# Kernel tuning notes

Hardware: AMD Instinct MI355X
Metric: run time of the kernel (lower is better)

## Reference

```python
import jax, jax.numpy as jnp
import numpy as np

H = 16
D_MODEL = 1024
D_K = D_MODEL // H
NEG = -1e9


def setup_inputs() -> dict:
    key = jax.random.key(0)
    ks = jax.random.split(key, 12)
    B, S = 2, 2048
    inp = {
        "query": jax.random.normal(ks[0], (B, S, D_MODEL), jnp.float32),
        "key": jax.random.normal(ks[1], (B, S, D_MODEL), jnp.float32),
        "value": jax.random.normal(ks[2], (B, S, D_MODEL), jnp.float32),
        "mask": jnp.ones((B, 1, S), jnp.int32),
    }
    s = 1.0 / np.sqrt(D_MODEL)
    for i, nm in enumerate(["Wq", "Wk", "Wv", "Wo"]):
        inp[nm] = jax.random.normal(ks[3 + i], (D_MODEL, D_MODEL), jnp.float32) * s
        inp["b" + nm[1]] = jax.random.normal(ks[7 + i], (D_MODEL,), jnp.float32) * s
    return inp


def _split_heads(x):
    B, S, _ = x.shape
    return x.reshape(B, S, H, D_K).transpose(0, 2, 1, 3)  # [B,H,S,Dk]


def reference(query, key, value, mask, Wq, bq, Wk, bk, Wv, bv, Wo, bo):
    q = _split_heads(query @ Wq + bq)
    k = _split_heads(key @ Wk + bk)
    v = _split_heads(value @ Wv + bv)
    scores = jnp.einsum("bhqd,bhkd->bhqk", q, k) / jnp.sqrt(jnp.float32(D_K))
    # mask [B,1,Sk] -> broadcast as [B,1,1,Sk]
    scores = jnp.where(mask[:, None, :, :] == 0, NEG, scores)
    attn = jax.nn.softmax(scores, axis=-1)  # dropout is identity in eval mode
    out = jnp.einsum("bhqk,bhkd->bhqd", attn, v)
    B, _, Sq, _ = out.shape
    out = out.transpose(0, 2, 1, 3).reshape(B, Sq, H * D_K)
    return out @ Wo + bo
```

## Files before the change

### kernel.cpp

```cpp
#include <hip/hip_runtime.h>
#include <hip/hip_bf16.h>

typedef __attribute__((ext_vector_type(8))) short short8;
typedef __attribute__((ext_vector_type(4))) float float4v;
typedef __attribute__((ext_vector_type(2))) unsigned int uint2v;
typedef __hip_bfloat16 bf16;

#define MFMA16(a, b, c) __builtin_amdgcn_mfma_f32_16x16x32_bf16((a), (b), (c), 0, 0, 0)

static __device__ __forceinline__ short8 load8(const bf16* p) {
    return *reinterpret_cast<const short8*>(p);
}
static __device__ __forceinline__ unsigned short bfu(float x) {
    union { bf16 b; unsigned short u; } c; c.b = __float2bfloat16(x); return c.u;
}
static __device__ __forceinline__ unsigned pack2(float lo, float hi) {
    return ((unsigned)bfu(hi) << 16) | bfu(lo);
}
static __device__ __forceinline__ short bf_bits(float x) {
    union { bf16 b; short u; } c; c.b = __float2bfloat16(x); return c.u;
}
static __device__ __forceinline__ short8 cvt8(float4 a, float4 b) {
    short8 r;
    r[0] = bf_bits(a.x); r[1] = bf_bits(a.y); r[2] = bf_bits(a.z); r[3] = bf_bits(a.w);
    r[4] = bf_bits(b.x); r[5] = bf_bits(b.y); r[6] = bf_bits(b.z); r[7] = bf_bits(b.w);
    return r;
}

typedef const __attribute__((address_space(1))) unsigned int* gp1;
typedef __attribute__((address_space(3))) unsigned int* lp3;
static __device__ __forceinline__ void async16(const void* g, void* l) {
    __builtin_amdgcn_global_load_lds((gp1)g, (lp3)l, 16, 0, 0);
}

__global__ __launch_bounds__(256) void transpose_qkv(
    const float* __restrict__ Wq, const float* __restrict__ Wk,
    const float* __restrict__ Wv, bf16* __restrict__ out_base)
{
    __shared__ bf16 tile[64][65];
    const float* in = (blockIdx.z == 0) ? Wq : (blockIdx.z == 1) ? Wk : Wv;
    bf16* out = out_base + (size_t)blockIdx.z * 1048576;
    int tx = threadIdx.x, ty = threadIdx.y;
    int bx = blockIdx.x * 64, by = blockIdx.y * 64;
    for (int i = ty; i < 64; i += 4)
        tile[i][tx] = __float2bfloat16(in[(size_t)(by + i) * 1024 + bx + tx]);
    __syncthreads();
    for (int i = ty; i < 64; i += 4)
        out[(size_t)(bx + i) * 1024 + by + tx] = tile[tx][i];
}

__global__ __launch_bounds__(256) void transpose_one(
    const float* __restrict__ in, bf16* __restrict__ out)
{
    __shared__ bf16 tile[64][65];
    int tx = threadIdx.x, ty = threadIdx.y;
    int bx = blockIdx.x * 64, by = blockIdx.y * 64;
    for (int i = ty; i < 64; i += 4)
        tile[i][tx] = __float2bfloat16(in[(size_t)(by + i) * 1024 + bx + tx]);
    __syncthreads();
    for (int i = ty; i < 64; i += 4)
        out[(size_t)(bx + i) * 1024 + by + tx] = tile[tx][i];
}

__global__ __launch_bounds__(256, 3) void qkv_gemm(
    const float* __restrict__ Xq, const float* __restrict__ Xk,
    const float* __restrict__ Xv, const bf16* __restrict__ Wt_all,
    const float* __restrict__ bq, const float* __restrict__ bk,
    const float* __restrict__ bv,
    bf16* __restrict__ outq, bf16* __restrict__ outk, bf16* __restrict__ outv)
{
    __shared__ float As[128 * 64];
    __shared__ bf16  Bs[128 * 64];

    int wg = blockIdx.x;
    int xcd = wg & 7;
    int jj = wg >> 3;
    int grp = xcd * 12 + (jj >> 3);
    int z = grp >> 5;
    int m_blk = grp & 31;
    int n_blk = jj & 7;

    const float* X    = (z == 0) ? Xq : (z == 1) ? Xk : Xv;
    const float* bias = (z == 0) ? bq : (z == 1) ? bk : bv;
    const bf16*  Wt   = Wt_all + (size_t)z * 1048576;
    bf16*        out  = (z == 0) ? outq : (z == 1) ? outk : outv;
    bool vmode = (z == 2);

    int tid = threadIdx.x;
    int w = tid >> 6, lane = tid & 63, l16 = lane & 15, quad = lane >> 4;
    int m_base = m_blk * 128, n_base = n_blk * 128;

    int r4 = lane >> 4, s16 = lane & 15;
    int r8 = lane >> 3, s8 = lane & 7;
    const float* Asrc0 = X + (size_t)(m_base + w * 32 + r4) * 1024 + ((s16 ^ r4) << 2);
    const float* Asrc1 = X + (size_t)(m_base + w * 32 + r4) * 1024 + ((s16 ^ (4 + r4)) << 2);
    const bf16*  Bsrc  = Wt + (size_t)(n_base + w * 32 + r8) * 1024 + ((s8 ^ r8) << 3);

    int wm = (w & 1) * 64, wn = (w >> 1) * 64;
    int sw = l16 & 7;

    float4v zero = {0.f, 0.f, 0.f, 0.f};
    float4v acc[4][4];
    #pragma unroll
    for (int mi = 0; mi < 4; ++mi)
        #pragma unroll
        for (int nj = 0; nj < 4; ++nj) acc[mi][nj] = zero;

    for (int it = 0; it < 16; ++it) {
        int kt = it * 64;
        #pragma unroll
        for (int p = 0; p < 8; ++p) {
            const float* s = ((p & 1) ? Asrc1 : Asrc0) + (size_t)p * 4096 + kt;
            async16(s, (char*)As + (w * 32 + p * 4) * 256);
        }
        #pragma unroll
        for (int p = 0; p < 4; ++p)
            async16(Bsrc + (size_t)p * 8192 + kt, (char*)Bs + (w * 32 + p * 8) * 128);
        __syncthreads();

        #pragma unroll
        for (int kk = 0; kk < 2; ++kk) {
            short8 af[4], bfr[4];
            #pragma unroll
            for (int mi = 0; mi < 4; ++mi) {
                const float* rp = As + (wm + mi * 16 + l16) * 64;
                float4 f0 = *(const float4*)(rp + (((kk * 8 + quad * 2)     ^ sw) << 2));
                float4 f1 = *(const float4*)(rp + (((kk * 8 + quad * 2 + 1) ^ sw) << 2));
                af[mi] = cvt8(f0, f1);
            }
            #pragma unroll
            for (int nj = 0; nj < 4; ++nj) {
                const bf16* rp = Bs + (wn + nj * 16 + l16) * 64;
                bfr[nj] = load8(rp + (((kk * 4 + quad) ^ sw) << 3));
            }
            #pragma unroll
            for (int mi = 0; mi < 4; ++mi)
                #pragma unroll
                for (int nj = 0; nj < 4; ++nj)
                    acc[mi][nj] = MFMA16(af[mi], bfr[nj], acc[mi][nj]);
        }
        __syncthreads();
    }

    float bsv[4];
    #pragma unroll
    for (int nj = 0; nj < 4; ++nj)
        bsv[nj] = bias[n_base + wn + nj * 16 + l16];

    float qs = (z == 0) ? 0.18033688f : 1.0f;

    #pragma unroll
    for (int mi = 0; mi < 4; ++mi) {
        #pragma unroll
        for (int nj = 0; nj < 4; ++nj) {
            int n = n_base + wn + nj * 16 + l16;
            int h = n >> 6, dk = n & 63;
            int m0 = m_base + wm + mi * 16 + quad * 4;
            int b = m0 >> 11, s0 = m0 & 2047;
            if (vmode) {
                float v0 = acc[mi][nj][0] + bsv[nj];
                float v1 = acc[mi][nj][1] + bsv[nj];
                float v2 = acc[mi][nj][2] + bsv[nj];
                float v3 = acc[mi][nj][3] + bsv[nj];
                uint2 pv; pv.x = pack2(v0, v1); pv.y = pack2(v2, v3);
                size_t idx = ((size_t)(b * 16 + h) * 64 + dk) * 2048 + s0;
                *reinterpret_cast<uint2*>(out + idx) = pv;
            } else {
                #pragma unroll
                for (int r = 0; r < 4; ++r) {
                    size_t idx = (((size_t)(b * 16 + h) * 2048 + s0 + r) * 64 + dk);
                    out[idx] = __float2bfloat16((acc[mi][nj][r] + bsv[nj]) * qs);
                }
            }
        }
    }
}

__global__ __launch_bounds__(256, 2) void out_gemm(
    const bf16* __restrict__ A, const bf16* __restrict__ Wt,
    const float* __restrict__ bias, float* __restrict__ out)
{
    __shared__ bf16 As[128 * 128];
    __shared__ bf16 Bs[64 * 128];

    int wg = blockIdx.x;
    int xcd = wg & 7;
    int jj = wg >> 3;
    int m_blk = xcd * 4 + (jj >> 4);
    int n_blk = jj & 15;

    int tid = threadIdx.x;
    int w = tid >> 6, lane = tid & 63, l16 = lane & 15, quad = lane >> 4;
    int m_base = m_blk * 128, n_base = n_blk * 64;

    int r4 = lane >> 4, s16 = lane & 15;

    int wm = (w & 1) * 64, wn = (w >> 1) * 32;

    float4v zero = {0.f, 0.f, 0.f, 0.f};
    float4v acc[4][2];
    #pragma unroll
    for (int mi = 0; mi < 4; ++mi)
        #pragma unroll
        for (int nj = 0; nj < 2; ++nj) acc[mi][nj] = zero;

    for (int it = 0; it < 8; ++it) {
        int kt = it * 128;
        #pragma unroll
        for (int p = 0; p < 8; ++p) {
            int row = w * 32 + p * 4 + r4;
            const bf16* s = A + (size_t)(m_base + row) * 1024 + kt
                              + ((s16 ^ (row & 15)) << 3);
            async16(s, (char*)As + (w * 32 + p * 4) * 256);
        }
        #pragma unroll
        for (int p = 0; p < 4; ++p) {
            int row = w * 16 + p * 4 + r4;
            const bf16* s = Wt + (size_t)(n_base + row) * 1024 + kt
                              + ((s16 ^ (row & 15)) << 3);
            async16(s, (char*)Bs + (w * 16 + p * 4) * 256);
        }
        __syncthreads();

        #pragma unroll
        for (int kk = 0; kk < 4; ++kk) {
            short8 af[4], bfr[2];
            #pragma unroll
            for (int mi = 0; mi < 4; ++mi) {
                const bf16* rp = As + (wm + mi * 16 + l16) * 128;
                af[mi] = load8(rp + (((kk * 4 + quad) ^ l16) << 3));
            }
            #pragma unroll
            for (int nj = 0; nj < 2; ++nj) {
                const bf16* rp = Bs + (wn + nj * 16 + l16) * 128;
                bfr[nj] = load8(rp + (((kk * 4 + quad) ^ l16) << 3));
            }
            #pragma unroll
            for (int mi = 0; mi < 4; ++mi)
                #pragma unroll
                for (int nj = 0; nj < 2; ++nj)
                    acc[mi][nj] = MFMA16(af[mi], bfr[nj], acc[mi][nj]);
        }
        __syncthreads();
    }

    float bsv[2];
    #pragma unroll
    for (int nj = 0; nj < 2; ++nj)
        bsv[nj] = bias[n_base + wn + nj * 16 + l16];

    #pragma unroll
    for (int mi = 0; mi < 4; ++mi)
        #pragma unroll
        for (int nj = 0; nj < 2; ++nj) {
            int n = n_base + wn + nj * 16 + l16;
            int m0 = m_base + wm + mi * 16 + quad * 4;
            #pragma unroll
            for (int r = 0; r < 4; ++r)
                out[(size_t)(m0 + r) * 1024 + n] = acc[mi][nj][r] + bsv[nj];
        }
}

__global__ __launch_bounds__(512, 4) void attn_fused(
    const bf16* __restrict__ Qm, const bf16* __restrict__ Km,
    const bf16* __restrict__ Vt, const int* __restrict__ mask,
    bf16* __restrict__ Oout)
{
    __shared__ __align__(16) bf16 Kc[3][64 * 64];
    __shared__ __align__(16) bf16 Vc[3][64 * 64];
    __shared__ unsigned long long maskb[32];

    int tid = threadIdx.x;
    int w = tid >> 6, lane = tid & 63, l16 = lane & 15, quad = lane >> 4;
    int wg = blockIdx.x;
    int xcd = wg & 7;
    int jj = wg >> 3;
    int bh = xcd * 4 + (jj >> 4);
    int qg = jj & 15;
    int b = bh >> 4, h = bh & 15;
    int qt = qg * 8 + w;

    const int* mb = mask + b * 2048;
    #pragma unroll
    for (int i = 0; i < 4; ++i) {
        unsigned long long bal = __ballot(mb[w * 256 + i * 64 + lane] != 0);
        if (lane == 0) maskb[w * 4 + i] = bal;
    }

    const bf16* Qb = Qm + ((size_t)bh * 2048 + (size_t)qt * 16) * 64;
    short8 bQ0 = load8(Qb + l16 * 64 + quad * 8);
    short8 bQ1 = load8(Qb + l16 * 64 + 32 + quad * 8);

    int r8 = lane >> 3, s8 = lane & 7;
    const bf16* Ksrc = Km + (size_t)bh * 131072 + (size_t)(w * 8 + r8) * 64 + ((s8 ^ r8) << 3);
    const bf16* Vsrc = Vt + (size_t)bh * 131072 + (size_t)(w * 8 + r8) * 2048 + ((s8 ^ r8) << 3);

    int sw = l16 & 7;

    float4v zero = {0.f, 0.f, 0.f, 0.f};
    float4v Oacc[4];
    #pragma unroll
    for (int g = 0; g < 4; ++g) Oacc[g] = zero;
    float lsum = 0.f;

    async16(Ksrc,        (char*)&Kc[0][0] + w * 1024);
    async16(Vsrc,        (char*)&Vc[0][0] + w * 1024);
    async16(Ksrc + 4096, (char*)&Kc[1][0] + w * 1024);
    async16(Vsrc + 64,   (char*)&Vc[1][0] + w * 1024);
    asm volatile("s_waitcnt vmcnt(2) lgkmcnt(0)" ::: "memory");
    __builtin_amdgcn_s_barrier();
    __builtin_amdgcn_sched_barrier(0);

    int cur = 0, sb = 2;
    for (int it = 0; it < 32; ++it) {
        if (it < 30) {
            async16(Ksrc + (size_t)(it + 2) * 4096, (char*)&Kc[sb][0] + w * 1024);
            async16(Vsrc + (size_t)(it + 2) * 64,   (char*)&Vc[sb][0] + w * 1024);
        }

        unsigned long long m64 = maskb[it];
        bool full = (m64 == ~0ull);
        const bf16* Kb = &Kc[cur][0];
        const bf16* Vb = &Vc[cur][0];

        float4v S[4];
        #pragma unroll
        for (int kj = 0; kj < 4; ++kj) {
            const bf16* kr = Kb + (kj * 16 + l16) * 64;
            short8 a0 = load8(kr + (((0 + quad) ^ sw) << 3));
            short8 a1 = load8(kr + (((4 + quad) ^ sw) << 3));
            float4v s = MFMA16(a0, bQ0, zero);
            s = MFMA16(a1, bQ1, s);
            S[kj] = s;
        }

        unsigned wlo[4], whi[4];
        #pragma unroll
        for (int kj = 0; kj < 4; ++kj) {
            unsigned m4 = (unsigned)(m64 >> (kj * 16 + quad * 4)) & 0xFu;
            float p[4];
            #pragma unroll
            for (int r = 0; r < 4; ++r)
                p[r] = __builtin_amdgcn_exp2f(S[kj][r]);
            if (!full) {
                #pragma unroll
                for (int r = 0; r < 4; ++r)
                    p[r] = ((m4 >> r) & 1u) ? p[r] : 0.f;
            }
            lsum += (p[0] + p[1]) + (p[2] + p[3]);
            wlo[kj] = pack2(p[0], p[1]);
            whi[kj] = pack2(p[2], p[3]);
        }

        short8 ap[2];
        #pragma unroll
        for (int m = 0; m < 2; ++m) {
            uint2v sa = __builtin_amdgcn_permlane32_swap(wlo[2 * m], wlo[2 * m + 1], false, false);
            uint2v qa = __builtin_amdgcn_permlane16_swap(sa[0], sa[1], false, false);
            uint2v sb2 = __builtin_amdgcn_permlane32_swap(whi[2 * m], whi[2 * m + 1], false, false);
            uint2v qb2 = __builtin_amdgcn_permlane16_swap(sb2[0], sb2[1], false, false);
            union { short8 s; unsigned u[4]; } t;
            t.u[0] = qa[0];
            t.u[1] = qb2[0];
            t.u[2] = qa[1];
            t.u[3] = qb2[1];
            ap[m] = t.s;
        }

        #pragma unroll
        for (int g = 0; g < 4; ++g) {
            const bf16* vr = Vb + (g * 16 + l16) * 64;
            short8 v0 = load8(vr + (((0 + quad) ^ sw) << 3));
            short8 v1 = load8(vr + (((4 + quad) ^ sw) << 3));
            Oacc[g] = MFMA16(ap[0], v0, Oacc[g]);
            Oacc[g] = MFMA16(ap[1], v1, Oacc[g]);
        }

        if (it < 30) {
            asm volatile("s_waitcnt vmcnt(2)" ::: "memory");
            __builtin_amdgcn_s_barrier();
            __builtin_amdgcn_sched_barrier(0);
        } else if (it == 30) {
            asm volatile("s_waitcnt vmcnt(0)" ::: "memory");
            __builtin_amdgcn_s_barrier();
            __builtin_amdgcn_sched_barrier(0);
        }
        cur = (cur == 2) ? 0 : cur + 1;
        sb  = (sb  == 2) ? 0 : sb + 1;
    }

    float ls = lsum;
    ls += __shfl_xor(ls, 16, 64);
    ls += __shfl_xor(ls, 32, 64);
    #pragma unroll
    for (int r = 0; r < 4; ++r) {
        float linv = 1.f / __shfl(ls, quad * 4 + r, 64);
        int srow = qt * 16 + quad * 4 + r;
        size_t base = ((size_t)b * 2048 + srow) * 1024 + h * 64;
        #pragma unroll
        for (int g = 0; g < 4; ++g)
            Oout[base + g * 16 + l16] = __float2bfloat16(Oacc[g][r] * linv);
    }
}

extern "C" void kernel_launch(void* const* d_in, const int* in_sizes, int n_in,
                              void* d_out, int out_size, void* d_ws, size_t ws_size,
                              hipStream_t stream) {
    const float* query = (const float*)d_in[0];
    const float* key   = (const float*)d_in[1];
    const float* value = (const float*)d_in[2];
    const int*   mask  = (const int*)d_in[3];
    const float* Wq = (const float*)d_in[4];
    const float* bq = (const float*)d_in[5];
    const float* Wk = (const float*)d_in[6];
    const float* bk = (const float*)d_in[7];
    const float* Wv = (const float*)d_in[8];
    const float* bv = (const float*)d_in[9];
    const float* Wo = (const float*)d_in[10];
    const float* bo = (const float*)d_in[11];

    char* ws = (char*)d_ws;
    const size_t MB = 1024 * 1024;
    bf16* vb     = (bf16*)ws;
    bf16* Wt_all = (bf16*)(ws + 8 * MB);
    bf16* aout   = (bf16*)(ws + 8 * MB);
    bf16* WtO    = (bf16*)ws;
    bf16* qb     = (bf16*)d_out;
    bf16* kb     = (bf16*)((char*)d_out + 8 * MB);
    float* out   = (float*)d_out;

    transpose_qkv<<<dim3(16, 16, 3), dim3(64, 4), 0, stream>>>(Wq, Wk, Wv, Wt_all);

    qkv_gemm<<<dim3(768), 256, 0, stream>>>(
        query, key, value, Wt_all, bq, bk, bv, qb, kb, vb);

    attn_fused<<<dim3(512), 512, 0, stream>>>(qb, kb, vb, mask, aout);

    transpose_one<<<dim3(16, 16), dim3(64, 4), 0, stream>>>(Wo, WtO);

    out_gemm<<<dim3(512), 256, 0, stream>>>(aout, WtO, bo, out);
}
```

Measured before the change: 239.5 us.

## Fuse weight transpose and bf16 conversion into GEMM B-tile loads

```diff
diff --git a/kernel.cpp b/kernel.cpp
--- a/kernel.cpp
+++ b/kernel.cpp
@@ -33,38 +33,11 @@
     __builtin_amdgcn_global_load_lds((gp1)g, (lp3)l, 16, 0, 0);
 }
 
-__global__ __launch_bounds__(256) void transpose_qkv(
-    const float* __restrict__ Wq, const float* __restrict__ Wk,
-    const float* __restrict__ Wv, bf16* __restrict__ out_base)
-{
-    __shared__ bf16 tile[64][65];
-    const float* in = (blockIdx.z == 0) ? Wq : (blockIdx.z == 1) ? Wk : Wv;
-    bf16* out = out_base + (size_t)blockIdx.z * 1048576;
-    int tx = threadIdx.x, ty = threadIdx.y;
-    int bx = blockIdx.x * 64, by = blockIdx.y * 64;
-    for (int i = ty; i < 64; i += 4)
-        tile[i][tx] = __float2bfloat16(in[(size_t)(by + i) * 1024 + bx + tx]);
-    __syncthreads();
-    for (int i = ty; i < 64; i += 4)
-        out[(size_t)(bx + i) * 1024 + by + tx] = tile[tx][i];
-}
-
-__global__ __launch_bounds__(256) void transpose_one(
-    const float* __restrict__ in, bf16* __restrict__ out)
-{
-    __shared__ bf16 tile[64][65];
-    int tx = threadIdx.x, ty = threadIdx.y;
-    int bx = blockIdx.x * 64, by = blockIdx.y * 64;
-    for (int i = ty; i < 64; i += 4)
-        tile[i][tx] = __float2bfloat16(in[(size_t)(by + i) * 1024 + bx + tx]);
-    __syncthreads();
-    for (int i = ty; i < 64; i += 4)
-        out[(size_t)(bx + i) * 1024 + by + tx] = tile[tx][i];
-}
-
 __global__ __launch_bounds__(256, 3) void qkv_gemm(
     const float* __restrict__ Xq, const float* __restrict__ Xk,
-    const float* __restrict__ Xv, const bf16* __restrict__ Wt_all,
+    const float* __restrict__ Xv,
+    const float* __restrict__ Wq, const float* __restrict__ Wk,
+    const float* __restrict__ Wv,
     const float* __restrict__ bq, const float* __restrict__ bk,
     const float* __restrict__ bv,
     bf16* __restrict__ outq, bf16* __restrict__ outk, bf16* __restrict__ outv)
@@ -81,8 +54,8 @@
     int n_blk = jj & 7;
 
     const float* X    = (z == 0) ? Xq : (z == 1) ? Xk : Xv;
+    const float* W    = (z == 0) ? Wq : (z == 1) ? Wk : Wv;
     const float* bias = (z == 0) ? bq : (z == 1) ? bk : bv;
-    const bf16*  Wt   = Wt_all + (size_t)z * 1048576;
     bf16*        out  = (z == 0) ? outq : (z == 1) ? outk : outv;
     bool vmode = (z == 2);
 
@@ -91,10 +64,15 @@
     int m_base = m_blk * 128, n_base = n_blk * 128;
 
     int r4 = lane >> 4, s16 = lane & 15;
-    int r8 = lane >> 3, s8 = lane & 7;
     const float* Asrc0 = X + (size_t)(m_base + w * 32 + r4) * 1024 + ((s16 ^ r4) << 2);
     const float* Asrc1 = X + (size_t)(m_base + w * 32 + r4) * 1024 + ((s16 ^ (4 + r4)) << 2);
-    const bf16*  Bsrc  = Wt + (size_t)(n_base + w * 32 + r8) * 1024 + ((s8 ^ r8) << 3);
+
+    int bp  = lane >> 3;
+    int bli = lane & 7;
+    const float* Wsrc = W + (size_t)(w * 16 + bp * 2) * 1024 + n_base + bli * 16;
+    int bslot = w * 2 + (bp >> 2);
+    int bwk   = (bp & 3) * 4;
+    char* bbase = (char*)Bs + bli * 2048 + bwk;
 
     int wm = (w & 1) * 64, wn = (w >> 1) * 64;
     int sw = l16 & 7;
@@ -113,9 +91,23 @@
             const float* s = ((p & 1) ? Asrc1 : Asrc0) + (size_t)p * 4096 + kt;
             async16(s, (char*)As + (w * 32 + p * 4) * 256);
         }
-        #pragma unroll
-        for (int p = 0; p < 4; ++p)
-            async16(Bsrc + (size_t)p * 8192 + kt, (char*)Bs + (w * 32 + p * 8) * 128);
+        {
+            const float* r0 = Wsrc + (size_t)kt * 1024;
+            const float* r1 = r0 + 1024;
+            float fa[16], fb[16];
+            *(float4*)(fa + 0)  = *(const float4*)(r0 + 0);
+            *(float4*)(fa + 4)  = *(const float4*)(r0 + 4);
+            *(float4*)(fa + 8)  = *(const float4*)(r0 + 8);
+            *(float4*)(fa + 12) = *(const float4*)(r0 + 12);
+            *(float4*)(fb + 0)  = *(const float4*)(r1 + 0);
+            *(float4*)(fb + 4)  = *(const float4*)(r1 + 4);
+            *(float4*)(fb + 8)  = *(const float4*)(r1 + 8);
+            *(float4*)(fb + 12) = *(const float4*)(r1 + 12);
+            #pragma unroll
+            for (int i = 0; i < 16; ++i)
+                *(unsigned*)(bbase + i * 128 + ((bslot ^ (i & 7)) << 4)) =
+                    pack2(fa[i], fb[i]);
+        }
         __syncthreads();
 
         #pragma unroll
@@ -177,7 +169,7 @@
 }
 
 __global__ __launch_bounds__(256, 2) void out_gemm(
-    const bf16* __restrict__ A, const bf16* __restrict__ Wt,
+    const bf16* __restrict__ A, const float* __restrict__ Wo,
     const float* __restrict__ bias, float* __restrict__ out)
 {
     __shared__ bf16 As[128 * 128];
@@ -195,6 +187,13 @@
 
     int r4 = lane >> 4, s16 = lane & 15;
 
+    int bp  = lane >> 2;
+    int bli = lane & 3;
+    const float* Wsrc = Wo + (size_t)(w * 32 + bp * 2) * 1024 + n_base + bli * 16;
+    int bslot = w * 4 + (bp >> 2);
+    int bwk   = (bp & 3) * 4;
+    char* bbase = (char*)Bs + bli * 4096 + bwk;
+
     int wm = (w & 1) * 64, wn = (w >> 1) * 32;
 
     float4v zero = {0.f, 0.f, 0.f, 0.f};
@@ -213,12 +212,22 @@
                               + ((s16 ^ (row & 15)) << 3);
             async16(s, (char*)As + (w * 32 + p * 4) * 256);
         }
-        #pragma unroll
-        for (int p = 0; p < 4; ++p) {
-            int row = w * 16 + p * 4 + r4;
-            const bf16* s = Wt + (size_t)(n_base + row) * 1024 + kt
-                              + ((s16 ^ (row & 15)) << 3);
-            async16(s, (char*)Bs + (w * 16 + p * 4) * 256);
+        {
+            const float* r0 = Wsrc + (size_t)kt * 1024;
+            const float* r1 = r0 + 1024;
+            float fa[16], fb[16];
+            *(float4*)(fa + 0)  = *(const float4*)(r0 + 0);
+            *(float4*)(fa + 4)  = *(const float4*)(r0 + 4);
+            *(float4*)(fa + 8)  = *(const float4*)(r0 + 8);
+            *(float4*)(fa + 12) = *(const float4*)(r0 + 12);
+            *(float4*)(fb + 0)  = *(const float4*)(r1 + 0);
+            *(float4*)(fb + 4)  = *(const float4*)(r1 + 4);
+            *(float4*)(fb + 8)  = *(const float4*)(r1 + 8);
+            *(float4*)(fb + 12) = *(const float4*)(r1 + 12);
+            #pragma unroll
+            for (int i = 0; i < 16; ++i)
+                *(unsigned*)(bbase + i * 256 + ((bslot ^ i) << 4)) =
+                    pack2(fa[i], fb[i]);
         }
         __syncthreads();
 
@@ -421,22 +430,16 @@
 
     char* ws = (char*)d_ws;
     const size_t MB = 1024 * 1024;
-    bf16* vb     = (bf16*)ws;
-    bf16* Wt_all = (bf16*)(ws + 8 * MB);
-    bf16* aout   = (bf16*)(ws + 8 * MB);
-    bf16* WtO    = (bf16*)ws;
-    bf16* qb     = (bf16*)d_out;
-    bf16* kb     = (bf16*)((char*)d_out + 8 * MB);
-    float* out   = (float*)d_out;
-
-    transpose_qkv<<<dim3(16, 16, 3), dim3(64, 4), 0, stream>>>(Wq, Wk, Wv, Wt_all);
+    bf16* vb   = (bf16*)ws;
+    bf16* aout = (bf16*)(ws + 8 * MB);
+    bf16* qb   = (bf16*)d_out;
+    bf16* kb   = (bf16*)((char*)d_out + 8 * MB);
+    float* out = (float*)d_out;
 
     qkv_gemm<<<dim3(768), 256, 0, stream>>>(
-        query, key, value, Wt_all, bq, bk, bv, qb, kb, vb);
+        query, key, value, Wq, Wk, Wv, bq, bk, bv, qb, kb, vb);
 
     attn_fused<<<dim3(512), 512, 0, stream>>>(qb, kb, vb, mask, aout);
 
-    transpose_one<<<dim3(16, 16), dim3(64, 4), 0, stream>>>(Wo, WtO);
-
-    out_gemm<<<dim3(512), 256, 0, stream>>>(aout, WtO, bo, out);
-}
+    out_gemm<<<dim3(512), 256, 0, stream>>>(aout, Wo, bo, out);
+}
```

Result: slower. 247.1 us (+3.2%).
